# Optimization experiments

Measured on AMD Instinct MI355X. Metric: run time of the kernel, lower is better.

The kernel has to match this reference:

```python
import jax, jax.numpy as jnp
import numpy as np
from jax.ops import segment_sum, segment_max

N = 20000      # nodes
DEG = 16       # incoming edges per node
E = N * DEG    # edges
IN = 128       # in_features
BOND = 16      # bond_features_dim
OUT = 128      # output_features
NUM_LAYERS = 3
LEAKY = 0.2
ELU_ALPHA = 1.0


def _lin_params(key, out_f, in_f):
    kw, kb = jax.random.split(key)
    s = 1.0 / np.sqrt(in_f)
    w = jax.random.uniform(kw, (out_f, in_f), jnp.float32, -s, s)
    b = jax.random.uniform(kb, (out_f,), jnp.float32, -s, s)
    return w, b


def setup_inputs() -> dict:
    key = jax.random.key(0)
    ks = jax.random.split(key, 20)
    atom_features = jax.random.normal(ks[0], (N, IN), jnp.float32)
    edge_src = jax.random.randint(ks[1], (E,), 0, N, jnp.int32)
    # every node receives exactly DEG edges (avoids the isolated-node bug path)
    edge_dst = jnp.repeat(jnp.arange(N, dtype=jnp.int32), DEG)
    bond_features = jax.random.normal(ks[2], (E, BOND), jnp.float32)

    v1_fc1_w, v1_fc1_b = _lin_params(ks[3], OUT, IN)
    v1_fc2_w, v1_fc2_b = _lin_params(ks[4], OUT, IN + BOND)
    v1_att_w, v1_att_b = _lin_params(ks[5], 1, 2 * OUT)
    v1_attend_w, v1_attend_b = _lin_params(ks[6], OUT, OUT)
    v1_gru_wih, v1_gru_bih = _lin_params(ks[7], 3 * OUT, OUT)
    v1_gru_whh, v1_gru_bhh = _lin_params(ks[8], 3 * OUT, OUT)

    v2_fc1_w, v2_fc1_b = _lin_params(ks[9], 1, 2 * OUT)
    v2_fc2_w, v2_fc2_b = _lin_params(ks[10], OUT, OUT)
    v2_gru_wih, v2_gru_bih = _lin_params(ks[11], 3 * OUT, OUT)
    v2_gru_whh, v2_gru_bhh = _lin_params(ks[12], 3 * OUT, OUT)

    lin_w, lin_b = _lin_params(ks[13], OUT, OUT)

    return dict(atom_features=atom_features, edge_src=edge_src, edge_dst=edge_dst,
                bond_features=bond_features,
                v1_fc1_w=v1_fc1_w, v1_fc1_b=v1_fc1_b, v1_fc2_w=v1_fc2_w, v1_fc2_b=v1_fc2_b,
                v1_att_w=v1_att_w, v1_att_b=v1_att_b, v1_attend_w=v1_attend_w, v1_attend_b=v1_attend_b,
                v1_gru_wih=v1_gru_wih, v1_gru_whh=v1_gru_whh, v1_gru_bih=v1_gru_bih, v1_gru_bhh=v1_gru_bhh,
                v2_fc1_w=v2_fc1_w, v2_fc1_b=v2_fc1_b, v2_fc2_w=v2_fc2_w, v2_fc2_b=v2_fc2_b,
                v2_gru_wih=v2_gru_wih, v2_gru_whh=v2_gru_whh, v2_gru_bih=v2_gru_bih, v2_gru_bhh=v2_gru_bhh,
                lin_w=lin_w, lin_b=lin_b)


def _linear(x, w, b):
    return x @ w.T + b


def _gru_cell(x, h, wih, whh, bih, bhh):
    gi = x @ wih.T + bih   # [N, 3*OUT]
    gh = h @ whh.T + bhh
    i_r, i_z, i_n = jnp.split(gi, 3, axis=-1)
    h_r, h_z, h_n = jnp.split(gh, 3, axis=-1)
    r = jax.nn.sigmoid(i_r + h_r)
    z = jax.nn.sigmoid(i_z + h_z)
    n = jnp.tanh(i_n + r * h_n)
    return (1.0 - z) * n + z * h


def _segment_softmax(logits, seg, n):
    m = segment_max(logits, seg, num_segments=n)
    ex = jnp.exp(logits - m[seg])
    den = segment_sum(ex, seg, num_segments=n)
    return ex / den[seg]


def reference(atom_features, edge_src, edge_dst, bond_features,
              v1_fc1_w, v1_fc1_b, v1_fc2_w, v1_fc2_b, v1_att_w, v1_att_b,
              v1_attend_w, v1_attend_b, v1_gru_wih, v1_gru_whh, v1_gru_bih, v1_gru_bhh,
              v2_fc1_w, v2_fc1_b, v2_fc2_w, v2_fc2_b,
              v2_gru_wih, v2_gru_whh, v2_gru_bih, v2_gru_bhh,
              lin_w, lin_b):
    n = atom_features.shape[0]
    lrelu = lambda x: jax.nn.leaky_relu(x, negative_slope=LEAKY)

    # ---- GATlayerV1 ----
    new_atom = lrelu(_linear(atom_features, v1_fc1_w, v1_fc1_b))           # [N, OUT]
    nbr_trans = _linear(new_atom, v1_attend_w, v1_attend_b)                # [N, OUT]
    nbr_in = jnp.concatenate([atom_features[edge_src], bond_features], axis=1)  # [E, IN+BOND]
    nbr = lrelu(_linear(nbr_in, v1_fc2_w, v1_fc2_b))                       # [E, OUT]
    pair = jnp.concatenate([new_atom[edge_dst], nbr], axis=1)              # [E, 2*OUT]
    logits = lrelu(_linear(pair, v1_att_w, v1_att_b))[:, 0]                # [E]
    score = _segment_softmax(logits, edge_dst, n)                          # [E]
    transform = segment_sum(score[:, None] * nbr_trans[edge_src], edge_dst, num_segments=n)
    ctx = jax.nn.elu(transform, alpha=ELU_ALPHA)
    h = _gru_cell(ctx, new_atom, v1_gru_wih, v1_gru_whh, v1_gru_bih, v1_gru_bhh)
    G_0 = new_atom

    all_tensors = [h]

    # ---- GATlayerV2 (shared weights across layers 2..NUM_LAYERS) ----
    for _ in range(NUM_LAYERS - 1):
        nt = _linear(h, v2_fc2_w, v2_fc2_b)                                # [N, OUT]
        pair2 = jnp.concatenate([h[edge_dst], h[edge_src]], axis=1)        # [E, 2*OUT]
        lg = lrelu(_linear(pair2, v2_fc1_w, v2_fc1_b))[:, 0]               # [E]
        sc = _segment_softmax(lg, edge_dst, n)
        tr = segment_sum(sc[:, None] * nt[edge_src], edge_dst, num_segments=n)
        ctx2 = jax.nn.elu(tr, alpha=ELU_ALPHA)
        h = _gru_cell(ctx2, h, v2_gru_wih, v2_gru_whh, v2_gru_bih, v2_gru_bhh)
        all_tensors.append(h)

    all_stack = jnp.stack(all_tensors)           # [NUM_LAYERS, N, OUT]
    averaged = all_stack.mean(axis=0)            # [N, OUT]
    output = jax.nn.gelu(_linear(averaged, lin_w, lin_b), approximate=False)
    return (output, all_stack, G_0, averaged)
```

## Files before the change

### kernel.cpp

```cpp
#include <hip/hip_runtime.h>
#include <math.h>

#define NN 20000
#define EE 320000

using short8 = __attribute__((ext_vector_type(8))) short;
using f32x4  = __attribute__((ext_vector_type(4))) float;
using u16x4  = __attribute__((ext_vector_type(4))) unsigned short;

__device__ __forceinline__ unsigned short f2bf(float x) {
    union { float f; unsigned u; } v; v.f = x;
    unsigned r = (v.u + 0x7fffu + ((v.u >> 16) & 1u)) >> 16;
    return (unsigned short)r;
}
__device__ __forceinline__ float bf2f(unsigned short b) {
    union { unsigned u; float f; } v; v.u = ((unsigned)b) << 16;
    return v.f;
}
__device__ __forceinline__ float sigmoidf_(float x) { return 1.f / (1.f + __expf(-x)); }
__device__ __forceinline__ float tanhf_(float x) {
    float e = __expf(-2.f * x);
    return (1.f - e) / (1.f + e);
}
__device__ __forceinline__ float lrelu_(float x) { return x > 0.f ? x : 0.2f * x; }
__device__ __forceinline__ float elu_(float x) { return x > 0.f ? x : __expf(x) - 1.f; }

struct PackDesc { const float* w; unsigned short* out; int O; int ldw; int mode; };
struct PackArgs { PackDesc d[10]; };

__global__ void k_pack(PackArgs args) {
    PackDesc d = args.d[blockIdx.y];
    int idx = blockIdx.x * 256 + threadIdx.x;
    if (d.mode == 1) {
        if (idx >= 512) return;
        int t = idx >> 6, l = idx & 63;
        int lr = l & 15, lg = l >> 4;
        int ch = lr * 8 + t;
        short8 o;
        #pragma unroll
        for (int j = 0; j < 8; j++) {
            int k = lg * 8 + j;
            o[j] = (k < 16) ? (short)f2bf(d.w[(size_t)ch * 144 + 128 + k]) : (short)0;
        }
        *(short8*)(d.out + (size_t)idx * 8) = o;
        return;
    }
    int total = (d.O / 16) * 4 * 64;
    if (idx >= total) return;
    int l = idx & 63, rest = idx >> 6;
    int ko = rest & 3, no = rest >> 2;
    int row = no * 16 + (l & 15);
    int col0 = ko * 32 + ((l >> 4) * 8);
    const float* src = d.w + (size_t)row * d.ldw + col0;
    unsigned short o[8];
    #pragma unroll
    for (int j = 0; j < 8; j++) o[j] = f2bf(src[j]);
    #pragma unroll
    for (int j = 0; j < 8; j++) d.out[(size_t)idx * 8 + j] = o[j];
}

__global__ __launch_bounds__(256) void k_v1_front(
    const float* __restrict__ atom,
    const unsigned short* __restrict__ Bfc1, const unsigned short* __restrict__ BW2a,
    const float* __restrict__ fc1_b, const float* __restrict__ fc2_b,
    const float* __restrict__ attw,
    float* __restrict__ g0, unsigned short* __restrict__ naBf,
    unsigned short* __restrict__ Ubf, float* __restrict__ adst)
{
    __shared__ float Xs[16][132];
    __shared__ unsigned short Ys2[16 * 128];
    const int tid = threadIdx.x, l = tid & 63, w = tid >> 6;
    const int lr = l & 15, lg = l >> 4;
    const int m0 = blockIdx.x * 16;

    f32x4 acc1[2] = {}, accU[2] = {};
    #pragma unroll
    for (int ko = 0; ko < 4; ko++) {
        const f32x4* ap = (const f32x4*)(atom + (size_t)(m0 + lr) * 128 + ko * 32 + lg * 8);
        f32x4 a0 = __builtin_nontemporal_load(ap);
        f32x4 a1 = __builtin_nontemporal_load(ap + 1);
        short8 af;
        #pragma unroll
        for (int j = 0; j < 4; j++) { af[j] = (short)f2bf(a0[j]); af[4 + j] = (short)f2bf(a1[j]); }
        #pragma unroll
        for (int i = 0; i < 2; i++) {
            int t = w * 2 + i;
            short8 b1 = *(const short8*)(Bfc1 + ((size_t)(t * 4 + ko) * 64 + l) * 8);
            acc1[i] = __builtin_amdgcn_mfma_f32_16x16x32_bf16(af, b1, acc1[i], 0, 0, 0);
            short8 bu = *(const short8*)(BW2a + ((size_t)(t * 4 + ko) * 64 + l) * 8);
            accU[i] = __builtin_amdgcn_mfma_f32_16x16x32_bf16(af, bu, accU[i], 0, 0, 0);
        }
    }
    #pragma unroll
    for (int i = 0; i < 2; i++) {
        int col = (w * 2 + i) * 16 + lr;
        float b1v = fc1_b[col], bUv = fc2_b[col];
        #pragma unroll
        for (int r = 0; r < 4; r++) {
            int row = lg * 4 + r;
            float v = lrelu_(acc1[i][r] + b1v);
            Xs[row][col] = v;
            Ys2[row * 128 + col] = f2bf(accU[i][r] + bUv);
        }
    }
    __syncthreads();
    *(short8*)(Ubf + (size_t)m0 * 128 + tid * 8) = *(const short8*)(Ys2 + tid * 8);
    {
        int row = tid >> 4, q = tid & 15;
        short8 tmp;
        float p = 0.f;
        float vv[8];
        #pragma unroll
        for (int j = 0; j < 8; j++) {
            float x = Xs[row][q * 8 + j];
            vv[j] = x;
            tmp[j] = (short)f2bf(x);
            p = fmaf(x, attw[q * 8 + j], p);
        }
        __builtin_nontemporal_store(*(f32x4*)vv,
            (f32x4*)(g0 + (size_t)(m0 + row) * 128 + q * 8));
        __builtin_nontemporal_store(*(f32x4*)(vv + 4),
            (f32x4*)(g0 + (size_t)(m0 + row) * 128 + q * 8 + 4));
        *(short8*)(naBf + (size_t)(m0 + row) * 128 + q * 8) = tmp;
        #pragma unroll
        for (int m = 1; m <= 8; m <<= 1) p += __shfl_xor(p, m, 16);
        if (q == 0) adst[m0 + row] = p;
    }
}

template<int AGGMODE, int FRONT, int FINAL>
__global__ __launch_bounds__(512, 4) void k_gru(
    const float* __restrict__ aD, const float* __restrict__ bS, const float* __restrict__ b1,
    const float* __restrict__ bond, const unsigned short* __restrict__ BW2b,
    const float* __restrict__ attw, const float* __restrict__ attb1,
    const float* __restrict__ adst, const unsigned short* __restrict__ U,
    const int* __restrict__ esrc, const unsigned short* __restrict__ V,
    const unsigned short* __restrict__ Bpre, const float* __restrict__ bpre,
    const unsigned short* __restrict__ Bih, const unsigned short* __restrict__ Bhh,
    const float* __restrict__ bih, const float* __restrict__ bhh,
    const unsigned short* __restrict__ hprevBf, float* __restrict__ houtF,
    unsigned short* __restrict__ houtBf,
    const float* __restrict__ w2att, float* __restrict__ aDOut, float* __restrict__ bSOut,
    const float* __restrict__ as0, const float* __restrict__ as1,
    const unsigned short* __restrict__ Blin, const float* __restrict__ linb,
    float* __restrict__ avgOut, float* __restrict__ outF)
{
    __shared__ unsigned short aggS[16][136];
    __shared__ unsigned short ctxS[16][136];
    __shared__ unsigned short hpS[16][136];
    __shared__ float lgS[(AGGMODE == 0) ? 16 : 1][16];
    const int tid = threadIdx.x, l = tid & 63, w = tid >> 6;
    const int lr = l & 15, lg = l >> 4;
    const int m0 = blockIdx.x * 16;
    const int r2 = tid >> 5, c4 = (tid & 31) * 4;

    *(u16x4*)&hpS[r2][c4] = *(const u16x4*)(hprevBf + (size_t)(m0 + r2) * 128 + c4);

    if (AGGMODE == 0) {
        float aw[8];
        #pragma unroll
        for (int t = 0; t < 8; t++) aw[t] = attw[128 + lr * 8 + t];
        const float ab = attb1[0];
        #pragma unroll
        for (int nn = 0; nn < 2; nn++) {
            const int n = m0 + w * 2 + nn;
            const int e0 = n * 16;
            short8 af = {};
            if (lg < 2) {
                const f32x4* bp = (const f32x4*)(bond + (size_t)(e0 + lr) * 16 + lg * 8);
                f32x4 b0 = __builtin_nontemporal_load(bp);
                f32x4 b1v = __builtin_nontemporal_load(bp + 1);
                #pragma unroll
                for (int j = 0; j < 4; j++) {
                    af[j] = (short)f2bf(b0[j]); af[4 + j] = (short)f2bf(b1v[j]);
                }
            }
            f32x4 c[8];
            #pragma unroll
            for (int t = 0; t < 8; t++) {
                short8 bw = *(const short8*)(BW2b + (size_t)(t * 64 + l) * 8);
                f32x4 z = {};
                c[t] = __builtin_amdgcn_mfma_f32_16x16x32_bf16(af, bw, z, 0, 0, 0);
            }
            float s[4];
            #pragma unroll
            for (int r = 0; r < 4; r++) {
                int e = e0 + lg * 4 + r;
                int src = esrc[e];
                short8 u = *(const short8*)(U + (size_t)src * 128 + lr * 8);
                float a0 = 0.f;
                #pragma unroll
                for (int t = 0; t < 8; t++)
                    a0 = fmaf(aw[t], lrelu_(c[t][r] + bf2f((unsigned short)u[t])), a0);
                s[r] = a0;
            }
            #pragma unroll
            for (int mk = 1; mk <= 8; mk <<= 1)
                #pragma unroll
                for (int r = 0; r < 4; r++) s[r] += __shfl_xor(s[r], mk, 16);
            if (lr == 0) {
                float anode = adst[n];
                #pragma unroll
                for (int r = 0; r < 4; r++)
                    lgS[w * 2 + nn][lg * 4 + r] = lrelu_(anode + ab + s[r]);
            }
        }
    }
    __syncthreads();

    const int g2 = tid >> 5;
    const int q2 = tid & 31;
    const int q = q2 & 15;
    const int hf = q2 >> 4;
    float wq;
    int srcq;
    {
        const int gnode = m0 + g2;
        const int e = gnode * 16 + q;
        srcq = esrc[e];
        float lgt;
        if (AGGMODE == 0) lgt = lgS[g2][q];
        else              lgt = lrelu_(aD[gnode] + bS[srcq] + b1[0]);
        float mx = lgt;
        #pragma unroll
        for (int mk = 1; mk <= 8; mk <<= 1) mx = fmaxf(mx, __shfl_xor(mx, mk, 16));
        float ex = __expf(lgt - mx);
        float den = ex;
        #pragma unroll
        for (int mk = 1; mk <= 8; mk <<= 1) den += __shfl_xor(den, mk, 16);
        wq = ex / den;
    }

    u16x4 gv[16];
    #pragma unroll
    for (int i = 0; i < 16; i++) {
        int si = __shfl(srcq, i, 16);
        gv[i] = *(const u16x4*)(V + (size_t)si * 128 + hf * 64 + q * 4);
    }

    f32x4 ah[3] = {};
    #pragma unroll
    for (int ko = 0; ko < 4; ko++) {
        short8 afh = *(const short8*)&hpS[lr][ko * 32 + lg * 8];
        #pragma unroll
        for (int g = 0; g < 3; g++) {
            short8 bh = *(const short8*)(Bhh + ((size_t)((w + 8 * g) * 4 + ko) * 64 + l) * 8);
            ah[g] = __builtin_amdgcn_mfma_f32_16x16x32_bf16(afh, bh, ah[g], 0, 0, 0);
        }
    }

    {
        float s[4] = {};
        #pragma unroll
        for (int i = 0; i < 16; i++) {
            float wi = __shfl(wq, i, 16);
            #pragma unroll
            for (int j = 0; j < 4; j++) s[j] = fmaf(wi, bf2f(gv[i][j]), s[j]);
        }
        u16x4 o;
        #pragma unroll
        for (int j = 0; j < 4; j++) o[j] = f2bf(s[j]);
        *(u16x4*)&aggS[g2][hf * 64 + q * 4] = o;
    }
    __syncthreads();

    f32x4 accp = {};
    #pragma unroll
    for (int ko = 0; ko < 4; ko++) {
        short8 afA = *(const short8*)&aggS[lr][ko * 32 + lg * 8];
        short8 bfp = *(const short8*)(Bpre + ((size_t)(w * 4 + ko) * 64 + l) * 8);
        accp = __builtin_amdgcn_mfma_f32_16x16x32_bf16(afA, bfp, accp, 0, 0, 0);
    }
    {
        const int col = w * 16 + lr;
        const float bb = bpre[col];
        #pragma unroll
        for (int r = 0; r < 4; r++)
            ctxS[lg * 4 + r][col] = f2bf(elu_(accp[r] + bb));
    }
    __syncthreads();

    f32x4 ai[3] = {};
    #pragma unroll
    for (int ko = 0; ko < 4; ko++) {
        short8 afc = *(const short8*)&ctxS[lr][ko * 32 + lg * 8];
        #pragma unroll
        for (int g = 0; g < 3; g++) {
            short8 bi = *(const short8*)(Bih + ((size_t)((w + 8 * g) * 4 + ko) * 64 + l) * 8);
            ai[g] = __builtin_amdgcn_mfma_f32_16x16x32_bf16(afc, bi, ai[g], 0, 0, 0);
        }
    }
    {
        const int c = w * 16 + lr;
        const float br = bih[c] + bhh[c];
        const float bz = bih[c + 128] + bhh[c + 128];
        const float bin_ = bih[c + 256];
        const float bhn = bhh[c + 256];
        #pragma unroll
        for (int r = 0; r < 4; r++) {
            const int lrow = lg * 4 + r;
            float rg = sigmoidf_(ai[0][r] + ah[0][r] + br);
            float zg = sigmoidf_(ai[1][r] + ah[1][r] + bz);
            float ng = tanhf_(ai[2][r] + bin_ + rg * (ah[2][r] + bhn));
            float hp = bf2f(hpS[lrow][c]);
            hpS[lrow][c] = f2bf(fmaf(zg, hp - ng, ng));
        }
    }
    __syncthreads();

    {
        u16x4 hv = *(const u16x4*)&hpS[r2][c4];
        f32x4 vf;
        #pragma unroll
        for (int j = 0; j < 4; j++) vf[j] = bf2f(hv[j]);
        __builtin_nontemporal_store(vf, (f32x4*)(houtF + (size_t)(m0 + r2) * 128 + c4));
        if (FINAL == 0)
            *(u16x4*)(houtBf + (size_t)(m0 + r2) * 128 + c4) = hv;
    }

    if (FRONT) {
        if (tid < 256) {
            int row = tid >> 4, qq = tid & 15;
            short8 hv8 = *(const short8*)&hpS[row][qq * 8];
            float pa = 0.f, pb = 0.f;
            #pragma unroll
            for (int j = 0; j < 8; j++) {
                float x = bf2f((unsigned short)hv8[j]);
                pa = fmaf(x, w2att[qq * 8 + j], pa);
                pb = fmaf(x, w2att[128 + qq * 8 + j], pb);
            }
            #pragma unroll
            for (int m = 1; m <= 8; m <<= 1) {
                pa += __shfl_xor(pa, m, 16);
                pb += __shfl_xor(pb, m, 16);
            }
            if (qq == 0) { aDOut[m0 + row] = pa; bSOut[m0 + row] = pb; }
        }
    }

    if (FINAL) {
        {
            f32x4 x0 = __builtin_nontemporal_load(
                (const f32x4*)(as0 + (size_t)(m0 + r2) * 128 + c4));
            f32x4 x1 = __builtin_nontemporal_load(
                (const f32x4*)(as1 + (size_t)(m0 + r2) * 128 + c4));
            u16x4 hv = *(const u16x4*)&hpS[r2][c4];
            f32x4 av;
            #pragma unroll
            for (int j = 0; j < 4; j++)
                av[j] = (x0[j] + x1[j] + bf2f(hv[j])) * (1.f / 3.f);
            __builtin_nontemporal_store(av, (f32x4*)(avgOut + (size_t)(m0 + r2) * 128 + c4));
            u16x4 ab16;
            #pragma unroll
            for (int j = 0; j < 4; j++) ab16[j] = f2bf(av[j]);
            *(u16x4*)&ctxS[r2][c4] = ab16;
        }
        __syncthreads();
        f32x4 acc2 = {};
        #pragma unroll
        for (int ko = 0; ko < 4; ko++) {
            short8 af = *(const short8*)&ctxS[lr][ko * 32 + lg * 8];
            short8 bf = *(const short8*)(Blin + ((size_t)(w * 4 + ko) * 64 + l) * 8);
            acc2 = __builtin_amdgcn_mfma_f32_16x16x32_bf16(af, bf, acc2, 0, 0, 0);
        }
        {
            const int col = w * 16 + lr;
            const float bb = linb[col];
            #pragma unroll
            for (int r = 0; r < 4; r++) {
                float vv = acc2[r] + bb;
                vv = 0.5f * vv * (1.f + erff(vv * 0.70710678118654752f));
                aggS[lg * 4 + r][col] = f2bf(vv);
            }
        }
        __syncthreads();
        {
            u16x4 ov = *(const u16x4*)&aggS[r2][c4];
            f32x4 vf;
            #pragma unroll
            for (int j = 0; j < 4; j++) vf[j] = bf2f(ov[j]);
            __builtin_nontemporal_store(vf, (f32x4*)(outF + (size_t)(m0 + r2) * 128 + c4));
        }
    }
}

extern "C" void kernel_launch(void* const* d_in, const int* in_sizes, int n_in,
                              void* d_out, int out_size, void* d_ws, size_t ws_size,
                              hipStream_t stream) {
    const float* atom     = (const float*)d_in[0];
    const int*   esrc     = (const int*)d_in[1];
    const float* bond     = (const float*)d_in[3];
    const float* fc1_w    = (const float*)d_in[4];
    const float* fc1_b    = (const float*)d_in[5];
    const float* fc2_w    = (const float*)d_in[6];
    const float* fc2_b    = (const float*)d_in[7];
    const float* att_w    = (const float*)d_in[8];
    const float* att_b    = (const float*)d_in[9];
    const float* attend_w = (const float*)d_in[10];
    const float* attend_b = (const float*)d_in[11];
    const float* gih1     = (const float*)d_in[12];
    const float* ghh1     = (const float*)d_in[13];
    const float* bih1     = (const float*)d_in[14];
    const float* bhh1     = (const float*)d_in[15];
    const float* fc1v2_w  = (const float*)d_in[16];
    const float* fc1v2_b  = (const float*)d_in[17];
    const float* fc2v2_w  = (const float*)d_in[18];
    const float* fc2v2_b  = (const float*)d_in[19];
    const float* gih2     = (const float*)d_in[20];
    const float* ghh2     = (const float*)d_in[21];
    const float* bih2     = (const float*)d_in[22];
    const float* bhh2     = (const float*)d_in[23];
    const float* lin_w    = (const float*)d_in[24];
    const float* lin_b    = (const float*)d_in[25];

    char* wsb = (char*)d_ws;
    size_t off = 0;
    auto allocB = [&](size_t bytes) {
        size_t o = off; off = (off + bytes + 255) & ~(size_t)255; return o;
    };
    unsigned short* Bfc1   = (unsigned short*)(wsb + allocB(128 * 128 * 2));
    unsigned short* Batt   = (unsigned short*)(wsb + allocB(128 * 128 * 2));
    unsigned short* BW2a   = (unsigned short*)(wsb + allocB(128 * 128 * 2));
    unsigned short* BW2b   = (unsigned short*)(wsb + allocB(512 * 8 * 2));
    unsigned short* Bgih1  = (unsigned short*)(wsb + allocB(384 * 128 * 2));
    unsigned short* Bghh1  = (unsigned short*)(wsb + allocB(384 * 128 * 2));
    unsigned short* Bfc2v2 = (unsigned short*)(wsb + allocB(128 * 128 * 2));
    unsigned short* Bgih2  = (unsigned short*)(wsb + allocB(384 * 128 * 2));
    unsigned short* Bghh2  = (unsigned short*)(wsb + allocB(384 * 128 * 2));
    unsigned short* Blin   = (unsigned short*)(wsb + allocB(128 * 128 * 2));
    unsigned short* naBf   = (unsigned short*)(wsb + allocB((size_t)NN * 128 * 2));
    unsigned short* Ubf    = (unsigned short*)(wsb + allocB((size_t)NN * 128 * 2));
    unsigned short* h1Bf   = (unsigned short*)(wsb + allocB((size_t)NN * 128 * 2));
    unsigned short* h2Bf   = (unsigned short*)(wsb + allocB((size_t)NN * 128 * 2));
    float* adst   = (float*)(wsb + allocB((size_t)NN * 4));
    float* aD     = (float*)(wsb + allocB((size_t)NN * 4));
    float* bS     = (float*)(wsb + allocB((size_t)NN * 4));
    (void)ws_size;

    float* out0 = (float*)d_out;
    float* as0  = out0 + (size_t)NN * 128;
    float* as1  = as0 + (size_t)NN * 128;
    float* as2  = as1 + (size_t)NN * 128;
    float* g0   = out0 + (size_t)4 * NN * 128;
    float* avg  = out0 + (size_t)5 * NN * 128;

    PackArgs pa;
    pa.d[0] = { fc1_w,    Bfc1,   128, 128, 0 };
    pa.d[1] = { attend_w, Batt,   128, 128, 0 };
    pa.d[2] = { fc2_w,    BW2a,   128, 144, 0 };
    pa.d[3] = { gih1,     Bgih1,  384, 128, 0 };
    pa.d[4] = { ghh1,     Bghh1,  384, 128, 0 };
    pa.d[5] = { fc2v2_w,  Bfc2v2, 128, 128, 0 };
    pa.d[6] = { gih2,     Bgih2,  384, 128, 0 };
    pa.d[7] = { ghh2,     Bghh2,  384, 128, 0 };
    pa.d[8] = { lin_w,    Blin,   128, 128, 0 };
    pa.d[9] = { fc2_w,    BW2b,   0,   0,   1 };
    k_pack<<<dim3(24, 10), 256, 0, stream>>>(pa);

    const int GB = NN / 16;

    k_v1_front<<<GB, 256, 0, stream>>>(atom, Bfc1, BW2a, fc1_b, fc2_b, att_w,
                                       g0, naBf, Ubf, adst);
    k_gru<0, 1, 0><<<GB, 512, 0, stream>>>(
        nullptr, nullptr, nullptr,
        bond, BW2b, att_w, att_b, adst, Ubf,
        esrc, naBf,
        Batt, attend_b,
        Bgih1, Bghh1, bih1, bhh1, naBf, as0, h1Bf,
        fc1v2_w, aD, bS,
        nullptr, nullptr, nullptr, nullptr, nullptr, nullptr);

    k_gru<1, 1, 0><<<GB, 512, 0, stream>>>(
        aD, bS, fc1v2_b,
        nullptr, nullptr, nullptr, nullptr, nullptr, nullptr,
        esrc, h1Bf,
        Bfc2v2, fc2v2_b,
        Bgih2, Bghh2, bih2, bhh2, h1Bf, as1, h2Bf,
        fc1v2_w, aD, bS,
        nullptr, nullptr, nullptr, nullptr, nullptr, nullptr);

    k_gru<1, 0, 1><<<GB, 512, 0, stream>>>(
        aD, bS, fc1v2_b,
        nullptr, nullptr, nullptr, nullptr, nullptr, nullptr,
        esrc, h2Bf,
        Bfc2v2, fc2v2_b,
        Bgih2, Bghh2, bih2, bhh2, h2Bf, as2, nullptr,
        nullptr, nullptr, nullptr,
        as0, as1, Blin, lin_b, avg, out0);
}
```

Baseline: 123.6 us.

## Store gathered node features in FP8 to halve gather traffic

```diff
diff --git a/kernel.cpp b/kernel.cpp
--- a/kernel.cpp
+++ b/kernel.cpp
@@ -6,6 +6,7 @@
 
 using short8 = __attribute__((ext_vector_type(8))) short;
 using f32x4  = __attribute__((ext_vector_type(4))) float;
+using f32x2  = __attribute__((ext_vector_type(2))) float;
 using u16x4  = __attribute__((ext_vector_type(4))) unsigned short;
 
 __device__ __forceinline__ unsigned short f2bf(float x) {
@@ -24,6 +25,18 @@
 }
 __device__ __forceinline__ float lrelu_(float x) { return x > 0.f ? x : 0.2f * x; }
 __device__ __forceinline__ float elu_(float x) { return x > 0.f ? x : __expf(x) - 1.f; }
+
+__device__ __forceinline__ unsigned pk_fp8x4(float a, float b, float c, float d) {
+    int w = 0;
+    w = __builtin_amdgcn_cvt_pk_fp8_f32(a, b, w, false);
+    w = __builtin_amdgcn_cvt_pk_fp8_f32(c, d, w, true);
+    return (unsigned)w;
+}
+__device__ __forceinline__ void up_fp8x4(unsigned w, float* o) {
+    f32x2 lo = __builtin_amdgcn_cvt_pk_f32_fp8((int)w, false);
+    f32x2 hi = __builtin_amdgcn_cvt_pk_f32_fp8((int)w, true);
+    o[0] = lo[0]; o[1] = lo[1]; o[2] = hi[0]; o[3] = hi[1];
+}
 
 struct PackDesc { const float* w; unsigned short* out; int O; int ldw; int mode; };
 struct PackArgs { PackDesc d[10]; };
@@ -65,7 +78,8 @@
     const float* __restrict__ fc1_b, const float* __restrict__ fc2_b,
     const float* __restrict__ attw,
     float* __restrict__ g0, unsigned short* __restrict__ naBf,
-    unsigned short* __restrict__ Ubf, float* __restrict__ adst)
+    unsigned char* __restrict__ naF8,
+    unsigned char* __restrict__ U8, float* __restrict__ adst)
 {
     __shared__ float Xs[16][132];
     __shared__ unsigned short Ys2[16 * 128];
@@ -104,7 +118,16 @@
         }
     }
     __syncthreads();
-    *(short8*)(Ubf + (size_t)m0 * 128 + tid * 8) = *(const short8*)(Ys2 + tid * 8);
+    {
+        short8 uy = *(const short8*)(Ys2 + tid * 8);
+        float uf[8];
+        #pragma unroll
+        for (int j = 0; j < 8; j++) uf[j] = bf2f((unsigned short)uy[j]);
+        uint2 o8;
+        o8.x = pk_fp8x4(uf[0], uf[1], uf[2], uf[3]);
+        o8.y = pk_fp8x4(uf[4], uf[5], uf[6], uf[7]);
+        *(uint2*)(U8 + (size_t)m0 * 128 + tid * 8) = o8;
+    }
     {
         int row = tid >> 4, q = tid & 15;
         short8 tmp;
@@ -122,6 +145,10 @@
         __builtin_nontemporal_store(*(f32x4*)(vv + 4),
             (f32x4*)(g0 + (size_t)(m0 + row) * 128 + q * 8 + 4));
         *(short8*)(naBf + (size_t)(m0 + row) * 128 + q * 8) = tmp;
+        uint2 n8;
+        n8.x = pk_fp8x4(vv[0], vv[1], vv[2], vv[3]);
+        n8.y = pk_fp8x4(vv[4], vv[5], vv[6], vv[7]);
+        *(uint2*)(naF8 + (size_t)(m0 + row) * 128 + q * 8) = n8;
         #pragma unroll
         for (int m = 1; m <= 8; m <<= 1) p += __shfl_xor(p, m, 16);
         if (q == 0) adst[m0 + row] = p;
@@ -133,13 +160,13 @@
     const float* __restrict__ aD, const float* __restrict__ bS, const float* __restrict__ b1,
     const float* __restrict__ bond, const unsigned short* __restrict__ BW2b,
     const float* __restrict__ attw, const float* __restrict__ attb1,
-    const float* __restrict__ adst, const unsigned short* __restrict__ U,
-    const int* __restrict__ esrc, const unsigned short* __restrict__ V,
+    const float* __restrict__ adst, const unsigned char* __restrict__ U8,
+    const int* __restrict__ esrc, const unsigned char* __restrict__ V8,
     const unsigned short* __restrict__ Bpre, const float* __restrict__ bpre,
     const unsigned short* __restrict__ Bih, const unsigned short* __restrict__ Bhh,
     const float* __restrict__ bih, const float* __restrict__ bhh,
     const unsigned short* __restrict__ hprevBf, float* __restrict__ houtF,
-    unsigned short* __restrict__ houtBf,
+    unsigned short* __restrict__ houtBf, unsigned char* __restrict__ houtF8,
     const float* __restrict__ w2att, float* __restrict__ aDOut, float* __restrict__ bSOut,
     const float* __restrict__ as0, const float* __restrict__ as1,
     const unsigned short* __restrict__ Blin, const float* __restrict__ linb,
@@ -187,11 +214,14 @@
             for (int r = 0; r < 4; r++) {
                 int e = e0 + lg * 4 + r;
                 int src = esrc[e];
-                short8 u = *(const short8*)(U + (size_t)src * 128 + lr * 8);
+                uint2 u2 = *(const uint2*)(U8 + (size_t)src * 128 + lr * 8);
+                float uf[8];
+                up_fp8x4(u2.x, uf);
+                up_fp8x4(u2.y, uf + 4);
                 float a0 = 0.f;
                 #pragma unroll
                 for (int t = 0; t < 8; t++)
-                    a0 = fmaf(aw[t], lrelu_(c[t][r] + bf2f((unsigned short)u[t])), a0);
+                    a0 = fmaf(aw[t], lrelu_(c[t][r] + uf[t]), a0);
                 s[r] = a0;
             }
             #pragma unroll
@@ -231,11 +261,11 @@
         wq = ex / den;
     }
 
-    u16x4 gv[16];
+    unsigned gv[16];
     #pragma unroll
     for (int i = 0; i < 16; i++) {
         int si = __shfl(srcq, i, 16);
-        gv[i] = *(const u16x4*)(V + (size_t)si * 128 + hf * 64 + q * 4);
+        gv[i] = *(const unsigned*)(V8 + (size_t)si * 128 + hf * 64 + q * 4);
     }
 
     f32x4 ah[3] = {};
@@ -254,8 +284,10 @@
         #pragma unroll
         for (int i = 0; i < 16; i++) {
             float wi = __shfl(wq, i, 16);
-            #pragma unroll
-            for (int j = 0; j < 4; j++) s[j] = fmaf(wi, bf2f(gv[i][j]), s[j]);
+            float d[4];
+            up_fp8x4(gv[i], d);
+            #pragma unroll
+            for (int j = 0; j < 4; j++) s[j] = fmaf(wi, d[j], s[j]);
         }
         u16x4 o;
         #pragma unroll
@@ -314,8 +346,11 @@
         #pragma unroll
         for (int j = 0; j < 4; j++) vf[j] = bf2f(hv[j]);
         __builtin_nontemporal_store(vf, (f32x4*)(houtF + (size_t)(m0 + r2) * 128 + c4));
-        if (FINAL == 0)
+        if (FINAL == 0) {
             *(u16x4*)(houtBf + (size_t)(m0 + r2) * 128 + c4) = hv;
+            *(unsigned*)(houtF8 + (size_t)(m0 + r2) * 128 + c4) =
+                pk_fp8x4(vf[0], vf[1], vf[2], vf[3]);
+        }
     }
 
     if (FRONT) {
@@ -429,9 +464,12 @@
     unsigned short* Bghh2  = (unsigned short*)(wsb + allocB(384 * 128 * 2));
     unsigned short* Blin   = (unsigned short*)(wsb + allocB(128 * 128 * 2));
     unsigned short* naBf   = (unsigned short*)(wsb + allocB((size_t)NN * 128 * 2));
-    unsigned short* Ubf    = (unsigned short*)(wsb + allocB((size_t)NN * 128 * 2));
     unsigned short* h1Bf   = (unsigned short*)(wsb + allocB((size_t)NN * 128 * 2));
     unsigned short* h2Bf   = (unsigned short*)(wsb + allocB((size_t)NN * 128 * 2));
+    unsigned char*  U8     = (unsigned char*)(wsb + allocB((size_t)NN * 128));
+    unsigned char*  naF8   = (unsigned char*)(wsb + allocB((size_t)NN * 128));
+    unsigned char*  h1F8   = (unsigned char*)(wsb + allocB((size_t)NN * 128));
+    unsigned char*  h2F8   = (unsigned char*)(wsb + allocB((size_t)NN * 128));
     float* adst   = (float*)(wsb + allocB((size_t)NN * 4));
     float* aD     = (float*)(wsb + allocB((size_t)NN * 4));
     float* bS     = (float*)(wsb + allocB((size_t)NN * 4));
@@ -460,31 +498,31 @@
     const int GB = NN / 16;
 
     k_v1_front<<<GB, 256, 0, stream>>>(atom, Bfc1, BW2a, fc1_b, fc2_b, att_w,
-                                       g0, naBf, Ubf, adst);
+                                       g0, naBf, naF8, U8, adst);
     k_gru<0, 1, 0><<<GB, 512, 0, stream>>>(
         nullptr, nullptr, nullptr,
-        bond, BW2b, att_w, att_b, adst, Ubf,
-        esrc, naBf,
+        bond, BW2b, att_w, att_b, adst, U8,
+        esrc, naF8,
         Batt, attend_b,
-        Bgih1, Bghh1, bih1, bhh1, naBf, as0, h1Bf,
+        Bgih1, Bghh1, bih1, bhh1, naBf, as0, h1Bf, h1F8,
         fc1v2_w, aD, bS,
         nullptr, nullptr, nullptr, nullptr, nullptr, nullptr);
 
     k_gru<1, 1, 0><<<GB, 512, 0, stream>>>(
         aD, bS, fc1v2_b,
         nullptr, nullptr, nullptr, nullptr, nullptr, nullptr,
-        esrc, h1Bf,
+        esrc, h1F8,
         Bfc2v2, fc2v2_b,
-        Bgih2, Bghh2, bih2, bhh2, h1Bf, as1, h2Bf,
+        Bgih2, Bghh2, bih2, bhh2, h1Bf, as1, h2Bf, h2F8,
         fc1v2_w, aD, bS,
         nullptr, nullptr, nullptr, nullptr, nullptr, nullptr);
 
     k_gru<1, 0, 1><<<GB, 512, 0, stream>>>(
         aD, bS, fc1v2_b,
         nullptr, nullptr, nullptr, nullptr, nullptr, nullptr,
-        esrc, h2Bf,
+        esrc, h2F8,
         Bfc2v2, fc2v2_b,
-        Bgih2, Bghh2, bih2, bhh2, h2Bf, as2, nullptr,
+        Bgih2, Bghh2, bih2, bhh2, h2Bf, as2, nullptr, nullptr,
         nullptr, nullptr, nullptr,
         as0, as1, Blin, lin_b, avg, out0);
 }
```

After: 113.6 us. -8.1%, faster.
